# Optimization experiments

Hardware: AMD Instinct MI355X
Metric: run time of the kernel (lower is better)

The kernel has to match this reference:

```python
import jax, jax.numpy as jnp
import numpy as np

B, SEQ, NF = 16, 512, 32
E, HID, PRED = 128, 512, 96
N_FFT, HOP, TOPM = 64, 32, 32
W = SEQ // HOP + 1          # 17 windows (centered STFT)
F = N_FFT // 2 + 1          # 33 onesided freqs
LAM = 0.01                  # sparsity_threshold (softshrink)
SCALE = 0.02


def _hann(n):
    # periodic hann, matches torch.hann_window default
    return 0.5 - 0.5 * jnp.cos(2.0 * jnp.pi * jnp.arange(n) / n)


def _softshrink(v):
    return jnp.sign(v) * jnp.maximum(jnp.abs(v) - LAM, 0.0)


def setup_inputs():
    key = jax.random.key(0)
    ks = jax.random.split(key, 12)
    d = {}
    d['x'] = jax.random.normal(ks[0], (B, SEQ, NF), jnp.float32)
    d['embeddings'] = jax.random.normal(ks[1], (1, E), jnp.float32)
    for nm, k in zip(['Wr', 'Wi', 'Wrl', 'Wil', 'Wrr', 'Wir'], ks[2:8]):
        d[nm] = SCALE * jax.random.normal(k, (W, E, E), jnp.float32)
    d['br'] = SCALE * jax.random.normal(ks[8], (W, E), jnp.float32)
    d['bi'] = SCALE * jax.random.normal(ks[9], (W, E), jnp.float32)
    d['fc_w1'] = SCALE * jax.random.normal(ks[10], (SEQ * E, HID), jnp.float32)
    d['fc_b1'] = jnp.zeros((HID,), jnp.float32)
    d['fc_w2'] = SCALE * jax.random.normal(ks[11], (HID, PRED), jnp.float32)
    d['fc_b2'] = jnp.zeros((PRED,), jnp.float32)
    return d


def _forward(x, embeddings, Wr, Wi, Wrl, Wil, Wrr, Wir, br, bi,
             fc_w1, fc_b1, fc_w2, fc_b2):
    Bq, T, N = x.shape
    # tokenEmb: (B,T,N) -> (B,N,T,E)
    xe = x.transpose(0, 2, 1)[..., None] * embeddings
    bias = xe
    # ---- STFT (centered, reflect pad, hann, onesided) ----
    xt = xe.transpose(0, 1, 3, 2)                      # (B,N,E,T)
    pad = N_FFT // 2
    xp = jnp.pad(xt, ((0, 0), (0, 0), (0, 0), (pad, pad)), mode='reflect')
    win = _hann(N_FFT).astype(x.dtype)
    idx = jnp.arange(W)[:, None] * HOP + jnp.arange(N_FFT)[None, :]  # (W,nfft)
    frames = xp[..., idx] * win                        # (B,N,E,W,nfft)
    spec = jnp.fft.rfft(frames, axis=-1)               # (B,N,E,W,F)
    spec = spec.transpose(0, 1, 3, 4, 2)               # (B,N,W,F,E)
    # ---- top-M frequency select (dim=3) ----
    sm = jnp.moveaxis(spec, 3, -1)                     # (B,N,W,E,F)
    _, top_idx = jax.lax.top_k(jnp.abs(sm), TOPM)      # (B,N,W,E,M)
    vals = jnp.take_along_axis(sm, top_idx, axis=-1)
    xw = jnp.moveaxis(vals, -1, 3)                     # (B,N,W,M,E)
    # ---- per-window complex MLP with left/right neighbor windows ----
    z0 = jnp.zeros_like(xw[:, :, :1])
    xl = jnp.concatenate([z0, xw[:, :, :-1]], axis=2)  # left neighbor (zero at w=0)
    xr = jnp.concatenate([xw[:, :, 1:], z0], axis=2)   # right neighbor (zero at w=W-1)

    def cmul(z, wr, wi):
        re = jnp.einsum('bnwme,wef->bnwmf', z.real, wr) - jnp.einsum('bnwme,wef->bnwmf', z.imag, wi)
        im = jnp.einsum('bnwme,wef->bnwmf', z.imag, wr) + jnp.einsum('bnwme,wef->bnwmf', z.real, wi)
        return re, im

    re_m, im_m = cmul(xw, Wr, Wi)
    re_l, im_l = cmul(xl, Wrl, Wil)
    re_r, im_r = cmul(xr, Wrr, Wir)
    o_re = jax.nn.relu(re_m + re_l + re_r + br[None, None, :, None, :])
    o_im = jax.nn.relu(im_m + im_l + im_r + bi[None, None, :, None, :])
    y = _softshrink(o_re) + 1j * _softshrink(o_im)     # (B,N,W,M,E) complex
    # ---- scatter-pad back to full frequency grid ----
    ym = jnp.moveaxis(y, 3, -1)                        # (B,N,W,E,M)
    K = Bq * N * W * E
    flat_vals = ym.reshape(K, TOPM)
    flat_idx = top_idx.reshape(K, TOPM)
    full = jnp.zeros((K, F), ym.dtype).at[jnp.arange(K)[:, None], flat_idx].set(flat_vals)
    spec_full = jnp.moveaxis(full.reshape(Bq, N, W, E, F), -1, 3)  # (B,N,W,F,E)
    # ---- ISTFT (windowed OLA / window-squared envelope, centered trim) ----
    sf = spec_full.transpose(0, 1, 4, 2, 3)            # (B,N,E,W,F)
    fr = jnp.fft.irfft(sf, n=N_FFT, axis=-1) * win     # (B,N,E,W,nfft)
    L = (W - 1) * HOP + N_FFT
    ola = jnp.zeros((Bq, N, E, L), fr.dtype).at[..., idx].add(fr)
    env = jnp.zeros((L,), win.dtype).at[idx].add(win * win)
    ola = ola / jnp.where(env > 1e-11, env, 1.0)
    xt2 = ola[..., pad:L - pad]                        # (B,N,E,T)
    xo = xt2.transpose(0, 1, 3, 2) + bias              # (B,N,T,E) + residual
    # ---- fc head ----
    h = xo.reshape(Bq, N, T * E)
    h = jax.nn.leaky_relu(h @ fc_w1 + fc_b1, 0.01)
    out = h @ fc_w2 + fc_b2                            # (B,N,PRED)
    return out.transpose(0, 2, 1)                      # (B,PRED,N)


def reference(x, embeddings, Wr, Wi, Wrl, Wil, Wrr, Wir, br, bi,
              fc_w1, fc_b1, fc_w2, fc_b2):
    return _forward(x, embeddings, Wr, Wi, Wrl, Wil, Wrr, Wir, br, bi,
                    fc_w1, fc_b1, fc_w2, fc_b2)
```

## Files before the change

kernel.cpp:

```cpp
#include <hip/hip_runtime.h>
#include <hip/hip_bf16.h>

#define LAM 0.01f

typedef __attribute__((ext_vector_type(8))) short v8s;
typedef __attribute__((ext_vector_type(4))) float v4f;

static __device__ __forceinline__ unsigned short f2bf(float f) {
    union { float f; unsigned int u; } v; v.f = f;
    unsigned int u = v.u;
    u += 0x7fffu + ((u >> 16) & 1u);
    return (unsigned short)(u >> 16);
}
static __device__ __forceinline__ float bf2f(unsigned short h) {
    union { unsigned int u; float f; } c; c.u = ((unsigned int)h) << 16;
    return c.f;
}
static __device__ __forceinline__ unsigned int pkbf(float a, float b) {
    union { __hip_bfloat162 h; unsigned int u; } c;
    c.h = __float22bfloat162_rn(float2{a, b});
    return c.u;
}

static __device__ __forceinline__ void async16(const void* g, void* l) {
    __builtin_amdgcn_global_load_lds(
        (const __attribute__((address_space(1))) unsigned int*)g,
        (__attribute__((address_space(3))) unsigned int*)l, 16, 0, 0);
}

#define OFF_COEF 0ull
#define OFF_AIMG 3411968ull
#define OFF_W1P  70520832ull
#define OFF_HP   137629696ull

__global__ __launch_bounds__(256) void pre_kernel(
    const float* __restrict__ w1, unsigned short* __restrict__ w1p,
    const float* __restrict__ emb,
    const float* __restrict__ Wr, const float* __restrict__ Wi,
    const float* __restrict__ Wrl, const float* __restrict__ Wil,
    const float* __restrict__ Wrr, const float* __restrict__ Wir,
    const float* __restrict__ br, const float* __restrict__ bi,
    float* __restrict__ coef)
{
    if (blockIdx.y == 4) {
        const int bx = blockIdx.x;
        if (bx >= 68) return;
        const int pair = bx * 2 + (threadIdx.x >> 7);
        const int w = pair >> 3, j = pair & 7, e = threadIdx.x & 127;
        float out;
        if (j < 6) {
            const float* Wj;
            switch (j) {
                case 0: Wj = Wr; break; case 1: Wj = Wi; break;
                case 2: Wj = Wrl; break; case 3: Wj = Wil; break;
                case 4: Wj = Wrr; break; default: Wj = Wir; break;
            }
            const float* p = Wj + (size_t)w * 16384 + e;
            float acc = 0.f;
            #pragma unroll 8
            for (int ep = 0; ep < 128; ++ep) acc = fmaf(emb[ep], p[ep * 128], acc);
            out = acc;
        } else if (j == 6) {
            out = br[w * 128 + e] - LAM;
        } else {
            out = bi[w * 128 + e] - LAM;
        }
        coef[((size_t)(w * 128 + e)) * 8 + j] = out;
        return;
    }

    __shared__ float T[32][132];
    const int kb = blockIdx.x, nt = blockIdx.y;
    const int tid = threadIdx.x;

    #pragma unroll
    for (int p = 0; p < 4; ++p) {
        int r = (tid >> 5) + p * 8;
        int c = (tid & 31) * 4;
        float4 v = *(const float4*)&w1[((size_t)(kb * 32 + r)) * 512 + nt * 128 + c];
        T[r][c] = v.x; T[r][c + 1] = v.y; T[r][c + 2] = v.z; T[r][c + 3] = v.w;
    }
    __syncthreads();

    unsigned short* dst = w1p + ((size_t)nt * 2048 + kb) * 4096;
    #pragma unroll
    for (int p = 0; p < 2; ++p) {
        int pos = tid + 256 * p;
        int np = pos >> 2, cs = pos & 3;
        int clog = cs ^ ((np >> 2) & 3);
        unsigned int pk[4];
        #pragma unroll
        for (int j2 = 0; j2 < 4; ++j2)
            pk[j2] = pkbf(T[clog * 8 + j2 * 2][np], T[clog * 8 + j2 * 2 + 1][np]);
        *(uint4*)&dst[pos * 8] = make_uint4(pk[0], pk[1], pk[2], pk[3]);
    }
}

#define MID_ROLL(J0, J1, J2, J3)                                                \
    {                                                                           \
        _Pragma("unroll") for (int e2 = 0; e2 < 2; ++e2)                        \
        _Pragma("unroll") for (int i = 0; i < 4; ++i) {                         \
            roll[e2][J0][i] = fmaf(acc[0][e2][i], win16[0][i], roll[e2][J0][i]);\
            roll[e2][J1][i] = fmaf(acc[1][e2][i], win16[1][i], roll[e2][J1][i]);\
            roll[e2][J2][i] = fmaf(acc[2][e2][i], win16[2][i], roll[e2][J2][i]);\
            roll[e2][J3][i] = fmaf(acc[3][e2][i], win16[3][i], roll[e2][J3][i]);\
        }                                                                       \
    }

#define MID_FLUSH(JJA, JJB)                                                     \
    {                                                                           \
        _Pragma("unroll") for (int i = 0; i < 4; ++i) {                         \
            int tp = 32 * (w - 1) + q * 4 + i;                                  \
            float xb = sig[tp + 32];                                            \
            _Pragma("unroll") for (int e2 = 0; e2 < 2; ++e2) {                  \
                float val = fmaf(roll[e2][JJA][i], renv[0][i], xb * emb2[e2]);  \
                Aimg[cbase[e2] + (size_t)tp * 16384] = f2bf(val);               \
                roll[e2][JJA][i] = 0.f;                                         \
            }                                                                   \
            int tp2 = tp + 16;                                                  \
            float xb2 = sig[tp2 + 32];                                          \
            _Pragma("unroll") for (int e2 = 0; e2 < 2; ++e2) {                  \
                float val = fmaf(roll[e2][JJB][i], renv[1][i], xb2 * emb2[e2]); \
                Aimg[cbase[e2] + (size_t)tp2 * 16384] = f2bf(val);              \
                roll[e2][JJB][i] = 0.f;                                         \
            }                                                                   \
        }                                                                       \
    }

__global__ __launch_bounds__(256) void stftmid_kernel(
    const float* __restrict__ x, const float* __restrict__ emb,
    const float* __restrict__ coef, unsigned short* __restrict__ Aimg)
{
    __shared__ unsigned short M1t[2][64 * 72];
    __shared__ unsigned short Yt[2][128 * 72];
    __shared__ float cosT[64];
    __shared__ float sinT[64];
    __shared__ float2 Vs2[19 * 32];
    __shared__ int Bns[17 * 32];
    __shared__ float sig[576];
    __shared__ float winT[64];
    __shared__ float2 tw[64];
    __shared__ float2 Sbuf[17 * 33];
    __shared__ float absb[17 * 33];

    const int blk = blockIdx.x;
    const int b = blk >> 5, n = blk & 31;
    const int tid = threadIdx.x;
    const int wave = tid >> 6, lane = tid & 63, l15 = lane & 15, q = lane >> 4;
    const float C64 = 0.09817477042468103f;

    if (tid < 64) {
        float ang = (float)tid * C64;
        winT[tid] = 0.5f - 0.5f * cosf(ang);
        tw[tid] = make_float2(cosf(ang), sinf(ang));
        cosT[tid] = __cosf(ang);
        sinT[tid] = __sinf(ang);
        int r = (tid < 32) ? tid : (18 * 32 + tid - 32);
        Vs2[r] = make_float2(0.f, 0.f);
    }
    for (int l = tid; l < 576; l += 256) {
        int t = (l < 32) ? (32 - l) : ((l < 544) ? (l - 32) : (1054 - l));
        sig[l] = x[(size_t)b * 16384 + t * 32 + n];
    }
    __syncthreads();

    for (int task = tid; task < 561; task += 256) {
        int w = task / 33, f = task - w * 33;
        float sr = 0.f, si = 0.f;
        int base = w * 32;
        for (int t = 0; t < 64; ++t) {
            float sw = sig[base + t] * winT[t];
            float2 cs = tw[(f * t) & 63];
            sr = fmaf(sw, cs.x, sr);
            si = fmaf(sw, -cs.y, si);
        }
        Sbuf[task] = make_float2(sr, si);
        absb[task] = sqrtf(fmaf(sr, sr, si * si));
    }
    __syncthreads();

    for (int task = tid; task < 561; task += 256) {
        int w = task / 33, f = task - w * 33;
        float a = absb[task];
        int base = w * 33, rank = 0;
        for (int j = 0; j < 33; ++j) {
            float aj = absb[base + j];
            rank += (aj > a) || (aj == a && j < f);
        }
        if (rank < 32) {
            Vs2[32 + w * 32 + rank] = Sbuf[task];
            Bns[w * 32 + rank] = f;
        }
    }

    float win16[4][4];
    #pragma unroll
    for (int tt = 0; tt < 4; ++tt)
        #pragma unroll
        for (int i = 0; i < 4; ++i) {
            int t = tt * 16 + q * 4 + i;
            win16[tt][i] = 0.5f - 0.5f * __cosf((float)t * C64);
        }
    float renv[2][4];
    #pragma unroll
    for (int hf = 0; hf < 2; ++hf)
        #pragma unroll
        for (int i = 0; i < 4; ++i) {
            int k = hf * 16 + q * 4 + i;
            float w0 = 0.5f - 0.5f * __cosf((float)k * C64);
            float w1v = 0.5f - 0.5f * __cosf((float)(k + 32) * C64);
            renv[hf][i] = 1.0f / (w0 * w0 + w1v * w1v);
        }
    int ebase[2];
    float emb2[2];
    size_t cbase[2];
    const int mt = blk >> 7, mp = blk & 127, s = (mp >> 2) & 3;
    #pragma unroll
    for (int e2 = 0; e2 < 2; ++e2) {
        ebase[e2] = (wave * 2 + e2) * 16 + l15;
        emb2[e2] = emb[ebase[e2]];
        int e = ebase[e2];
        int echunk = e >> 5, clog = (e >> 3) & 3, cs = clog ^ s, el = e & 7;
        cbase[e2] = ((size_t)mt * 2048 + echunk) * 4096 + mp * 32 + cs * 8 + el;
    }

    float roll[2][4][4];
    #pragma unroll
    for (int e2 = 0; e2 < 2; ++e2)
        #pragma unroll
        for (int jj = 0; jj < 4; ++jj)
            #pragma unroll
            for (int i = 0; i < 4; ++i) roll[e2][jj][i] = 0.f;

    const int e1 = tid & 127;
    const int mg = (tid >> 7) << 4;
    const int tM = tid & 63;
    const int kg = wave << 4;

    __syncthreads();

    for (int w = 0; w < 17; ++w) {
        const int buf = w & 1;
        {
            const float4* cf = (const float4*)(coef + ((size_t)(w * 128 + e1)) * 8);
            float4 cA = cf[0];
            float4 cB = cf[1];
            unsigned int rep[8], imp[8];
            #pragma unroll
            for (int j2 = 0; j2 < 8; ++j2) {
                float rev[2], imv[2];
                #pragma unroll
                for (int sdx = 0; sdx < 2; ++sdx) {
                    int m = mg + j2 * 2 + sdx;
                    float2 vm = Vs2[(w + 1) * 32 + m];
                    float2 vl = Vs2[w * 32 + m];
                    float2 vp = Vs2[(w + 2) * 32 + m];
                    float re = cB.z;
                    re = fmaf(vm.x, cA.x, re); re = fmaf(-vm.y, cA.y, re);
                    re = fmaf(vl.x, cA.z, re); re = fmaf(-vl.y, cA.w, re);
                    re = fmaf(vp.x, cB.x, re); re = fmaf(-vp.y, cB.y, re);
                    float im = cB.w;
                    im = fmaf(vm.y, cA.x, im); im = fmaf(vm.x, cA.y, im);
                    im = fmaf(vl.y, cA.z, im); im = fmaf(vl.x, cA.w, im);
                    im = fmaf(vp.y, cB.x, im); im = fmaf(vp.x, cB.y, im);
                    rev[sdx] = fmaxf(re, 0.f);
                    imv[sdx] = fmaxf(im, 0.f);
                }
                rep[j2] = pkbf(rev[0], rev[1]);
                imp[j2] = pkbf(imv[0], imv[1]);
            }
            uint4* dr = (uint4*)&Yt[buf][e1 * 72 + mg];
            dr[0] = make_uint4(rep[0], rep[1], rep[2], rep[3]);
            dr[1] = make_uint4(rep[4], rep[5], rep[6], rep[7]);
            uint4* di = (uint4*)&Yt[buf][e1 * 72 + 32 + mg];
            di[0] = make_uint4(imp[0], imp[1], imp[2], imp[3]);
            di[1] = make_uint4(imp[4], imp[5], imp[6], imp[7]);
        }
        {
            unsigned int mpk[8];
            #pragma unroll
            for (int j2 = 0; j2 < 8; ++j2) {
                float vv[2];
                #pragma unroll
                for (int sdx = 0; sdx < 2; ++sdx) {
                    int k = kg + j2 * 2 + sdx;
                    int m = k & 31;
                    int r = Bns[w * 32 + m];
                    float sc = (r == 0 || r == 32) ? 0.015625f : 0.03125f;
                    int idx = (r * tM) & 63;
                    vv[sdx] = (k < 32) ? (cosT[idx] * sc) : (-sinT[idx] * sc);
                }
                mpk[j2] = pkbf(vv[0], vv[1]);
            }
            uint4* dm = (uint4*)&M1t[buf][tM * 72 + kg];
            dm[0] = make_uint4(mpk[0], mpk[1], mpk[2], mpk[3]);
            dm[1] = make_uint4(mpk[4], mpk[5], mpk[6], mpk[7]);
        }
        __syncthreads();

        v4f acc[4][2];
        #pragma unroll
        for (int tt = 0; tt < 4; ++tt)
            #pragma unroll
            for (int e2 = 0; e2 < 2; ++e2) acc[tt][e2] = (v4f){0.f, 0.f, 0.f, 0.f};
        #pragma unroll
        for (int ks = 0; ks < 2; ++ks) {
            v8s bfr[2];
            #pragma unroll
            for (int e2 = 0; e2 < 2; ++e2)
                bfr[e2] = *(const v8s*)&Yt[buf][ebase[e2] * 72 + ks * 32 + q * 8];
            #pragma unroll
            for (int tt = 0; tt < 4; ++tt) {
                v8s af = *(const v8s*)&M1t[buf][(tt * 16 + l15) * 72 + ks * 32 + q * 8];
                #pragma unroll
                for (int e2 = 0; e2 < 2; ++e2)
                    acc[tt][e2] = __builtin_amdgcn_mfma_f32_16x16x32_bf16(
                        af, bfr[e2], acc[tt][e2], 0, 0, 0);
            }
        }

        if ((w & 1) == 0) {
            MID_ROLL(0, 1, 2, 3);
            if (w > 0) {
                MID_FLUSH(0, 1);
            } else {
                #pragma unroll
                for (int e2 = 0; e2 < 2; ++e2)
                    #pragma unroll
                    for (int i = 0; i < 4; ++i) {
                        roll[e2][0][i] = 0.f; roll[e2][1][i] = 0.f;
                    }
            }
        } else {
            MID_ROLL(2, 3, 0, 1);
            MID_FLUSH(2, 3);
        }
    }
}

__global__ __launch_bounds__(512) void gemm_kernel(
    const unsigned short* __restrict__ Aimg, const unsigned short* __restrict__ w1p,
    unsigned short* __restrict__ hp, int iters, int KS)
{
    __shared__ unsigned short As[3][8192];
    __shared__ unsigned short Bs[3][8192];

    const int gid = blockIdx.x;
    const int xcd = gid & 7;
    const int u = gid >> 3;
    const int KS4 = KS >> 2;
    const int nt2 = (u >= KS4) ? 1 : 0;
    const int vv = u - nt2 * KS4;
    const int pid = vv * 8 + xcd;
    const int ks = pid >> 1;
    const int mt2 = pid & 1;

    const int tid = threadIdx.x;
    const int wave = tid >> 6, lane = tid & 63;
    const int l15 = lane & 15, q = lane >> 4;
    const int kb0 = ks * iters;

    const int isB = wave >> 2;
    const int sub = wave & 3;
    const unsigned short* gsrc = (isB
        ? w1p + ((size_t)(nt2 * 2 + (sub >> 1)) * 2048 + kb0) * 4096
        : Aimg + ((size_t)(mt2 * 2 + (sub >> 1)) * 2048 + kb0) * 4096)
        + (sub & 1) * 2048 + lane * 8;
    const int ldsoff = (sub >> 1) * 4096 + (sub & 1) * 2048;

    v4f acc[4][8];
    #pragma unroll
    for (int mf = 0; mf < 4; ++mf)
        #pragma unroll
        for (int nf = 0; nf < 8; ++nf) acc[mf][nf] = (v4f){0.f, 0.f, 0.f, 0.f};

    {
        unsigned short* dst0 = (isB ? Bs[0] : As[0]) + ldsoff;
        #pragma unroll
        for (int j = 0; j < 4; ++j) async16(gsrc + j * 512, dst0 + j * 512);
        if (iters > 1) {
            const unsigned short* s1 = gsrc + 4096;
            unsigned short* dst1 = (isB ? Bs[1] : As[1]) + ldsoff;
            #pragma unroll
            for (int j = 0; j < 4; ++j) async16(s1 + j * 512, dst1 + j * 512);
        }
    }

    const int wm = wave >> 1, wn = wave & 1;
    const int ca = (q ^ ((l15 >> 2) & 3)) * 8;
    const int rA = (wm >> 1) * 4096 + ((wm & 1) * 64 + l15) * 32 + ca;
    const int rB = wn * 4096 + l15 * 32 + ca;

    for (int it = 0; it < iters; ++it) {
        if (it + 1 < iters) {
            asm volatile("s_waitcnt vmcnt(4)" ::: "memory");
        } else {
            asm volatile("s_waitcnt vmcnt(0)" ::: "memory");
        }
        __builtin_amdgcn_s_barrier();
        __builtin_amdgcn_sched_barrier(0);
        if (it + 2 < iters) {
            const int nb = (it + 2) % 3;
            const unsigned short* src = gsrc + (size_t)(it + 2) * 4096;
            unsigned short* dst = (isB ? Bs[nb] : As[nb]) + ldsoff;
            #pragma unroll
            for (int j = 0; j < 4; ++j) async16(src + j * 512, dst + j * 512);
        }
        const int cur = it % 3;
        v8s af[4], bf[8];
        #pragma unroll
        for (int f = 0; f < 4; ++f) af[f] = *(const v8s*)&As[cur][rA + f * 512];
        #pragma unroll
        for (int nf = 0; nf < 8; ++nf) bf[nf] = *(const v8s*)&Bs[cur][rB + nf * 512];
        #pragma unroll
        for (int mf = 0; mf < 4; ++mf)
            #pragma unroll
            for (int nf = 0; nf < 8; ++nf)
                acc[mf][nf] = __builtin_amdgcn_mfma_f32_16x16x32_bf16(
                    af[mf], bf[nf], acc[mf][nf], 0, 0, 0);
    }

    #pragma unroll
    for (int mf = 0; mf < 4; ++mf)
        #pragma unroll
        for (int nf = 0; nf < 8; ++nf) {
            int row = mt2 * 256 + wm * 64 + mf * 16 + q * 4;
            int col = nt2 * 256 + wn * 128 + nf * 16 + l15;
            unsigned short* dst = hp + ((size_t)row * KS + ks) * 512 + col;
            #pragma unroll
            for (int i = 0; i < 4; ++i)
                dst[(size_t)i * KS * 512] = f2bf(acc[mf][nf][i]);
        }
}

__global__ __launch_bounds__(256) void fc2_kernel(
    const unsigned short* __restrict__ hp, const float* __restrict__ b1,
    const float* __restrict__ w2, const float* __restrict__ b2,
    float* __restrict__ out, int KS)
{
    __shared__ float hbuf[512];
    __shared__ float part[2][96];
    const int row = blockIdx.x;
    const int tid = threadIdx.x;

    const unsigned int* base = (const unsigned int*)(hp + (size_t)row * KS * 512) + tid;
    float a0 = 0.f, a1 = 0.f;
    #pragma unroll 8
    for (int k = 0; k < KS; ++k) {
        unsigned int v = base[k * 256];
        a0 += bf2f((unsigned short)(v & 0xffff));
        a1 += bf2f((unsigned short)(v >> 16));
    }
    float s0 = a0 + b1[tid * 2];
    float s1 = a1 + b1[tid * 2 + 1];
    hbuf[tid * 2]     = (s0 > 0.f) ? s0 : 0.01f * s0;
    hbuf[tid * 2 + 1] = (s1 > 0.f) ? s1 : 0.01f * s1;
    __syncthreads();

    if (tid < 192) {
        const int c = (tid >= 96) ? 1 : 0;
        const int o = tid - 96 * c;
        float a = 0.f;
        #pragma unroll 8
        for (int h = c * 256; h < c * 256 + 256; ++h)
            a = fmaf(hbuf[h], w2[h * 96 + o], a);
        part[c][o] = a;
    }
    __syncthreads();

    if (tid < 96) {
        float a = part[0][tid] + part[1][tid] + b2[tid];
        int b = row >> 5, n = row & 31;
        out[(size_t)b * 3072 + tid * 32 + n] = a;
    }
}

extern "C" void kernel_launch(void* const* d_in, const int* in_sizes, int n_in,
                              void* d_out, int out_size, void* d_ws, size_t ws_size,
                              hipStream_t stream) {
    const float* x   = (const float*)d_in[0];
    const float* emb = (const float*)d_in[1];
    const float* Wr  = (const float*)d_in[2];
    const float* Wi  = (const float*)d_in[3];
    const float* Wrl = (const float*)d_in[4];
    const float* Wil = (const float*)d_in[5];
    const float* Wrr = (const float*)d_in[6];
    const float* Wir = (const float*)d_in[7];
    const float* br  = (const float*)d_in[8];
    const float* bi  = (const float*)d_in[9];
    const float* w1  = (const float*)d_in[10];
    const float* b1  = (const float*)d_in[11];
    const float* w2  = (const float*)d_in[12];
    const float* b2  = (const float*)d_in[13];

    char* ws = (char*)d_ws;
    float* coef          = (float*)(ws + OFF_COEF);
    unsigned short* Aimg = (unsigned short*)(ws + OFF_AIMG);
    unsigned short* w1p  = (unsigned short*)(ws + OFF_W1P);
    unsigned short* hpp  = (unsigned short*)(ws + OFF_HP);

    int KS = 64;
    size_t hp_bytes = (size_t)KS * 512 * 512 * 2;
    if (OFF_HP + hp_bytes > ws_size) {
        KS = 32; hp_bytes = (size_t)KS * 512 * 512 * 2;
    }
    int iters = 2048 / KS;

    pre_kernel<<<dim3(2048, 5), dim3(256), 0, stream>>>(
        w1, w1p, emb, Wr, Wi, Wrl, Wil, Wrr, Wir, br, bi, coef);
    stftmid_kernel<<<dim3(512), dim3(256), 0, stream>>>(x, emb, coef, Aimg);
    gemm_kernel<<<dim3(4 * KS), dim3(512), 0, stream>>>(Aimg, w1p, hpp, iters, KS);
    fc2_kernel<<<dim3(512), dim3(256), 0, stream>>>(hpp, b1, w2, b2, (float*)d_out, KS);
}
```

Measured before the change: 435.2 us.

## Split STFT/top-k into separate kernel and single-buffer mid kernel LDS

Moves the STFT and top-32 frequency selection out of the fused mid kernel into its own kernel, which writes the selected spectrum values and bin indices to workspace. The mid kernel then reloads them. It also drops double-buffering of the Yt/M1t tiles in favour of a trailing barrier each window, and sets launch_bounds(256,4). The goal is to cut LDS and register use so more blocks fit per CU, at the cost of an extra launch, a global round trip, and an extra sync per window.

```diff
diff --git a/kernel.cpp b/kernel.cpp
--- a/kernel.cpp
+++ b/kernel.cpp
@@ -29,6 +29,8 @@
 }
 
 #define OFF_COEF 0ull
+#define OFF_V    69632ull
+#define OFF_BINS 2297856ull
 #define OFF_AIMG 3411968ull
 #define OFF_W1P  70520832ull
 #define OFF_HP   137629696ull
@@ -96,6 +98,62 @@
     }
 }
 
+__global__ __launch_bounds__(256) void stft_kernel(
+    const float* __restrict__ x, float2* __restrict__ V, int* __restrict__ bins)
+{
+    __shared__ float sig[576];
+    __shared__ float winT[64];
+    __shared__ float2 tw[64];
+    __shared__ float2 Sbuf[17 * 33];
+    __shared__ float absb[17 * 33];
+
+    const int blk = blockIdx.x;
+    const int b = blk >> 5, n = blk & 31;
+    const int tid = threadIdx.x;
+    const float C64 = 0.09817477042468103f;
+
+    if (tid < 64) {
+        float ang = (float)tid * C64;
+        winT[tid] = 0.5f - 0.5f * cosf(ang);
+        tw[tid] = make_float2(cosf(ang), sinf(ang));
+    }
+    for (int l = tid; l < 576; l += 256) {
+        int t = (l < 32) ? (32 - l) : ((l < 544) ? (l - 32) : (1054 - l));
+        sig[l] = x[(size_t)b * 16384 + t * 32 + n];
+    }
+    __syncthreads();
+
+    for (int task = tid; task < 561; task += 256) {
+        int w = task / 33, f = task - w * 33;
+        float sr = 0.f, si = 0.f;
+        int base = w * 32;
+        for (int t = 0; t < 64; ++t) {
+            float sw = sig[base + t] * winT[t];
+            float2 cs = tw[(f * t) & 63];
+            sr = fmaf(sw, cs.x, sr);
+            si = fmaf(sw, -cs.y, si);
+        }
+        Sbuf[task] = make_float2(sr, si);
+        absb[task] = sqrtf(fmaf(sr, sr, si * si));
+    }
+    __syncthreads();
+
+    for (int task = tid; task < 561; task += 256) {
+        int w = task / 33, f = task - w * 33;
+        float a = absb[task];
+        int base = w * 33, rank = 0;
+        for (int j = 0; j < 33; ++j) {
+            float aj = absb[base + j];
+            rank += (aj > a) || (aj == a && j < f);
+        }
+        if (rank < 32) {
+            size_t o = ((size_t)blk * 17 + w) * 32 + rank;
+            V[o] = Sbuf[task];
+            bins[o] = f;
+        }
+    }
+}
+
 #define MID_ROLL(J0, J1, J2, J3)                                                \
     {                                                                           \
         _Pragma("unroll") for (int e2 = 0; e2 < 2; ++e2)                        \
@@ -111,14 +169,14 @@
     {                                                                           \
         _Pragma("unroll") for (int i = 0; i < 4; ++i) {                         \
             int tp = 32 * (w - 1) + q * 4 + i;                                  \
-            float xb = sig[tp + 32];                                            \
+            float xb = xs[tp];                                                  \
             _Pragma("unroll") for (int e2 = 0; e2 < 2; ++e2) {                  \
                 float val = fmaf(roll[e2][JJA][i], renv[0][i], xb * emb2[e2]);  \
                 Aimg[cbase[e2] + (size_t)tp * 16384] = f2bf(val);               \
                 roll[e2][JJA][i] = 0.f;                                         \
             }                                                                   \
             int tp2 = tp + 16;                                                  \
-            float xb2 = sig[tp2 + 32];                                          \
+            float xb2 = xs[tp2];                                                \
             _Pragma("unroll") for (int e2 = 0; e2 < 2; ++e2) {                  \
                 float val = fmaf(roll[e2][JJB][i], renv[1][i], xb2 * emb2[e2]); \
                 Aimg[cbase[e2] + (size_t)tp2 * 16384] = f2bf(val);              \
@@ -127,21 +185,18 @@
         }                                                                       \
     }
 
-__global__ __launch_bounds__(256) void stftmid_kernel(
+__global__ __launch_bounds__(256, 4) void mid_kernel(
     const float* __restrict__ x, const float* __restrict__ emb,
-    const float* __restrict__ coef, unsigned short* __restrict__ Aimg)
+    const float* __restrict__ coef, const float2* __restrict__ V,
+    const int* __restrict__ bins, unsigned short* __restrict__ Aimg)
 {
-    __shared__ unsigned short M1t[2][64 * 72];
-    __shared__ unsigned short Yt[2][128 * 72];
+    __shared__ unsigned short M1t[64 * 72];
+    __shared__ unsigned short Yt[128 * 72];
     __shared__ float cosT[64];
     __shared__ float sinT[64];
     __shared__ float2 Vs2[19 * 32];
     __shared__ int Bns[17 * 32];
-    __shared__ float sig[576];
-    __shared__ float winT[64];
-    __shared__ float2 tw[64];
-    __shared__ float2 Sbuf[17 * 33];
-    __shared__ float absb[17 * 33];
+    __shared__ float xs[512];
 
     const int blk = blockIdx.x;
     const int b = blk >> 5, n = blk & 31;
@@ -151,46 +206,18 @@
 
     if (tid < 64) {
         float ang = (float)tid * C64;
-        winT[tid] = 0.5f - 0.5f * cosf(ang);
-        tw[tid] = make_float2(cosf(ang), sinf(ang));
         cosT[tid] = __cosf(ang);
         sinT[tid] = __sinf(ang);
-        int r = (tid < 32) ? tid : (18 * 32 + tid - 32);
-        Vs2[r] = make_float2(0.f, 0.f);
-    }
-    for (int l = tid; l < 576; l += 256) {
-        int t = (l < 32) ? (32 - l) : ((l < 544) ? (l - 32) : (1054 - l));
-        sig[l] = x[(size_t)b * 16384 + t * 32 + n];
-    }
-    __syncthreads();
-
-    for (int task = tid; task < 561; task += 256) {
-        int w = task / 33, f = task - w * 33;
-        float sr = 0.f, si = 0.f;
-        int base = w * 32;
-        for (int t = 0; t < 64; ++t) {
-            float sw = sig[base + t] * winT[t];
-            float2 cs = tw[(f * t) & 63];
-            sr = fmaf(sw, cs.x, sr);
-            si = fmaf(sw, -cs.y, si);
-        }
-        Sbuf[task] = make_float2(sr, si);
-        absb[task] = sqrtf(fmaf(sr, sr, si * si));
-    }
-    __syncthreads();
-
-    for (int task = tid; task < 561; task += 256) {
-        int w = task / 33, f = task - w * 33;
-        float a = absb[task];
-        int base = w * 33, rank = 0;
-        for (int j = 0; j < 33; ++j) {
-            float aj = absb[base + j];
-            rank += (aj > a) || (aj == a && j < f);
-        }
-        if (rank < 32) {
-            Vs2[32 + w * 32 + rank] = Sbuf[task];
-            Bns[w * 32 + rank] = f;
-        }
+    }
+    {
+        const float2* Vg = V + (size_t)blk * 544;
+        const int* Bg = bins + (size_t)blk * 544;
+        for (int i = tid; i < 544; i += 256) { Vs2[32 + i] = Vg[i]; Bns[i] = Bg[i]; }
+        if (tid < 64) {
+            int r = (tid < 32) ? tid : (18 * 32 + tid - 32);
+            Vs2[r] = make_float2(0.f, 0.f);
+        }
+        for (int i = tid; i < 512; i += 256) xs[i] = x[(size_t)b * 16384 + i * 32 + n];
     }
 
     float win16[4][4];
@@ -240,61 +267,63 @@
     __syncthreads();
 
     for (int w = 0; w < 17; ++w) {
-        const int buf = w & 1;
         {
             const float4* cf = (const float4*)(coef + ((size_t)(w * 128 + e1)) * 8);
             float4 cA = cf[0];
             float4 cB = cf[1];
-            unsigned int rep[8], imp[8];
-            #pragma unroll
-            for (int j2 = 0; j2 < 8; ++j2) {
-                float rev[2], imv[2];
+            #pragma unroll
+            for (int half = 0; half < 2; ++half) {
+                unsigned int rep[4], imp[4];
                 #pragma unroll
-                for (int sdx = 0; sdx < 2; ++sdx) {
-                    int m = mg + j2 * 2 + sdx;
-                    float2 vm = Vs2[(w + 1) * 32 + m];
-                    float2 vl = Vs2[w * 32 + m];
-                    float2 vp = Vs2[(w + 2) * 32 + m];
-                    float re = cB.z;
-                    re = fmaf(vm.x, cA.x, re); re = fmaf(-vm.y, cA.y, re);
-                    re = fmaf(vl.x, cA.z, re); re = fmaf(-vl.y, cA.w, re);
-                    re = fmaf(vp.x, cB.x, re); re = fmaf(-vp.y, cB.y, re);
-                    float im = cB.w;
-                    im = fmaf(vm.y, cA.x, im); im = fmaf(vm.x, cA.y, im);
-                    im = fmaf(vl.y, cA.z, im); im = fmaf(vl.x, cA.w, im);
-                    im = fmaf(vp.y, cB.x, im); im = fmaf(vp.x, cB.y, im);
-                    rev[sdx] = fmaxf(re, 0.f);
-                    imv[sdx] = fmaxf(im, 0.f);
+                for (int j2 = 0; j2 < 4; ++j2) {
+                    float rev[2], imv[2];
+                    #pragma unroll
+                    for (int sdx = 0; sdx < 2; ++sdx) {
+                        int m = mg + half * 8 + j2 * 2 + sdx;
+                        float2 vm = Vs2[(w + 1) * 32 + m];
+                        float2 vl = Vs2[w * 32 + m];
+                        float2 vp = Vs2[(w + 2) * 32 + m];
+                        float re = cB.z;
+                        re = fmaf(vm.x, cA.x, re); re = fmaf(-vm.y, cA.y, re);
+                        re = fmaf(vl.x, cA.z, re); re = fmaf(-vl.y, cA.w, re);
+                        re = fmaf(vp.x, cB.x, re); re = fmaf(-vp.y, cB.y, re);
+                        float im = cB.w;
+                        im = fmaf(vm.y, cA.x, im); im = fmaf(vm.x, cA.y, im);
+                        im = fmaf(vl.y, cA.z, im); im = fmaf(vl.x, cA.w, im);
+                        im = fmaf(vp.y, cB.x, im); im = fmaf(vp.x, cB.y, im);
+                        rev[sdx] = fmaxf(re, 0.f);
+                        imv[sdx] = fmaxf(im, 0.f);
+                    }
+                    rep[j2] = pkbf(rev[0], rev[1]);
+                    imp[j2] = pkbf(imv[0], imv[1]);
                 }
-                rep[j2] = pkbf(rev[0], rev[1]);
-                imp[j2] = pkbf(imv[0], imv[1]);
+                ((uint4*)&Yt[e1 * 72 + mg])[half] =
+                    make_uint4(rep[0], rep[1], rep[2], rep[3]);
+                ((uint4*)&Yt[e1 * 72 + 32 + mg])[half] =
+                    make_uint4(imp[0], imp[1], imp[2], imp[3]);
             }
-            uint4* dr = (uint4*)&Yt[buf][e1 * 72 + mg];
-            dr[0] = make_uint4(rep[0], rep[1], rep[2], rep[3]);
-            dr[1] = make_uint4(rep[4], rep[5], rep[6], rep[7]);
-            uint4* di = (uint4*)&Yt[buf][e1 * 72 + 32 + mg];
-            di[0] = make_uint4(imp[0], imp[1], imp[2], imp[3]);
-            di[1] = make_uint4(imp[4], imp[5], imp[6], imp[7]);
         }
         {
-            unsigned int mpk[8];
-            #pragma unroll
-            for (int j2 = 0; j2 < 8; ++j2) {
-                float vv[2];
+            #pragma unroll
+            for (int half = 0; half < 2; ++half) {
+                unsigned int mpk[4];
                 #pragma unroll
-                for (int sdx = 0; sdx < 2; ++sdx) {
-                    int k = kg + j2 * 2 + sdx;
-                    int m = k & 31;
-                    int r = Bns[w * 32 + m];
-                    float sc = (r == 0 || r == 32) ? 0.015625f : 0.03125f;
-                    int idx = (r * tM) & 63;
-                    vv[sdx] = (k < 32) ? (cosT[idx] * sc) : (-sinT[idx] * sc);
+                for (int j2 = 0; j2 < 4; ++j2) {
+                    float vv[2];
+                    #pragma unroll
+                    for (int sdx = 0; sdx < 2; ++sdx) {
+                        int k = kg + half * 8 + j2 * 2 + sdx;
+                        int m = k & 31;
+                        int r = Bns[w * 32 + m];
+                        float sc = (r == 0 || r == 32) ? 0.015625f : 0.03125f;
+                        int idx = (r * tM) & 63;
+                        vv[sdx] = (k < 32) ? (cosT[idx] * sc) : (-sinT[idx] * sc);
+                    }
+                    mpk[j2] = pkbf(vv[0], vv[1]);
                 }
-                mpk[j2] = pkbf(vv[0], vv[1]);
+                ((uint4*)&M1t[tM * 72 + kg])[half] =
+                    make_uint4(mpk[0], mpk[1], mpk[2], mpk[3]);
             }
-            uint4* dm = (uint4*)&M1t[buf][tM * 72 + kg];
-            dm[0] = make_uint4(mpk[0], mpk[1], mpk[2], mpk[3]);
-            dm[1] = make_uint4(mpk[4], mpk[5], mpk[6], mpk[7]);
         }
         __syncthreads();
 
@@ -308,10 +337,10 @@
             v8s bfr[2];
             #pragma unroll
             for (int e2 = 0; e2 < 2; ++e2)
-                bfr[e2] = *(const v8s*)&Yt[buf][ebase[e2] * 72 + ks * 32 + q * 8];
+                bfr[e2] = *(const v8s*)&Yt[ebase[e2] * 72 + ks * 32 + q * 8];
             #pragma unroll
             for (int tt = 0; tt < 4; ++tt) {
-                v8s af = *(const v8s*)&M1t[buf][(tt * 16 + l15) * 72 + ks * 32 + q * 8];
+                v8s af = *(const v8s*)&M1t[(tt * 16 + l15) * 72 + ks * 32 + q * 8];
                 #pragma unroll
                 for (int e2 = 0; e2 < 2; ++e2)
                     acc[tt][e2] = __builtin_amdgcn_mfma_f32_16x16x32_bf16(
@@ -335,6 +364,7 @@
             MID_ROLL(2, 3, 0, 1);
             MID_FLUSH(2, 3);
         }
+        if (w < 16) __syncthreads();
     }
 }
 
@@ -495,6 +525,8 @@
 
     char* ws = (char*)d_ws;
     float* coef          = (float*)(ws + OFF_COEF);
+    float2* V            = (float2*)(ws + OFF_V);
+    int* bins            = (int*)(ws + OFF_BINS);
     unsigned short* Aimg = (unsigned short*)(ws + OFF_AIMG);
     unsigned short* w1p  = (unsigned short*)(ws + OFF_W1P);
     unsigned short* hpp  = (unsigned short*)(ws + OFF_HP);
@@ -508,7 +540,8 @@
 
     pre_kernel<<<dim3(2048, 5), dim3(256), 0, stream>>>(
         w1, w1p, emb, Wr, Wi, Wrl, Wil, Wrr, Wir, br, bi, coef);
-    stftmid_kernel<<<dim3(512), dim3(256), 0, stream>>>(x, emb, coef, Aimg);
+    stft_kernel<<<dim3(512), dim3(256), 0, stream>>>(x, V, bins);
+    mid_kernel<<<dim3(512), dim3(256), 0, stream>>>(x, emb, coef, V, bins, Aimg);
     gemm_kernel<<<dim3(4 * KS), dim3(512), 0, stream>>>(Aimg, w1p, hpp, iters, KS);
     fc2_kernel<<<dim3(512), dim3(256), 0, stream>>>(hpp, b1, w2, b2, (float*)d_out, KS);
 }
```

Measured after the change: 398.8 us. 1.09x faster.

## Move STFT and top-k selection into idle pre_kernel blocks

Applied to the files above, without the earlier changes.

The forward STFT and per-window top-32 frequency ranking move out of the mid kernel into otherwise idle blocks of pre_kernel's y=4 row. Each (b,n) pair is split across two blocks by window halves. Results go to global V/bins buffers that mid_kernel loads, and mid_kernel keeps only a small residual signal buffer. The aim is to overlap this serial per-block work with the w1 repacking and to shorten mid_kernel, at the cost of a global round-trip and extra workspace.

```diff
diff --git a/kernel.cpp b/kernel.cpp
--- a/kernel.cpp
+++ b/kernel.cpp
@@ -29,6 +29,8 @@
 }
 
 #define OFF_COEF 0ull
+#define OFF_V    69632ull
+#define OFF_BINS 2297856ull
 #define OFF_AIMG 3411968ull
 #define OFF_W1P  70520832ull
 #define OFF_HP   137629696ull
@@ -40,38 +42,100 @@
     const float* __restrict__ Wrl, const float* __restrict__ Wil,
     const float* __restrict__ Wrr, const float* __restrict__ Wir,
     const float* __restrict__ br, const float* __restrict__ bi,
-    float* __restrict__ coef)
+    float* __restrict__ coef,
+    const float* __restrict__ x, float2* __restrict__ V, int* __restrict__ bins)
 {
+    __shared__ float T[32][132];
+    __shared__ float sigL[336];
+    __shared__ float winT[64];
+    __shared__ float2 tw[64];
+    __shared__ float2 Sbuf[9 * 33];
+    __shared__ float absb[9 * 33];
+
+    const int tid = threadIdx.x;
+
     if (blockIdx.y == 4) {
         const int bx = blockIdx.x;
-        if (bx >= 68) return;
-        const int pair = bx * 2 + (threadIdx.x >> 7);
-        const int w = pair >> 3, j = pair & 7, e = threadIdx.x & 127;
-        float out;
-        if (j < 6) {
-            const float* Wj;
-            switch (j) {
-                case 0: Wj = Wr; break; case 1: Wj = Wi; break;
-                case 2: Wj = Wrl; break; case 3: Wj = Wil; break;
-                case 4: Wj = Wrr; break; default: Wj = Wir; break;
-            }
-            const float* p = Wj + (size_t)w * 16384 + e;
-            float acc = 0.f;
-            #pragma unroll 8
-            for (int ep = 0; ep < 128; ++ep) acc = fmaf(emb[ep], p[ep * 128], acc);
-            out = acc;
-        } else if (j == 6) {
-            out = br[w * 128 + e] - LAM;
-        } else {
-            out = bi[w * 128 + e] - LAM;
-        }
-        coef[((size_t)(w * 128 + e)) * 8 + j] = out;
+        if (bx < 68) {
+            const int pair = bx * 2 + (tid >> 7);
+            const int w = pair >> 3, j = pair & 7, e = tid & 127;
+            float out;
+            if (j < 6) {
+                const float* Wj;
+                switch (j) {
+                    case 0: Wj = Wr; break; case 1: Wj = Wi; break;
+                    case 2: Wj = Wrl; break; case 3: Wj = Wil; break;
+                    case 4: Wj = Wrr; break; default: Wj = Wir; break;
+                }
+                const float* p = Wj + (size_t)w * 16384 + e;
+                float acc = 0.f;
+                #pragma unroll 8
+                for (int ep = 0; ep < 128; ++ep) acc = fmaf(emb[ep], p[ep * 128], acc);
+                out = acc;
+            } else if (j == 6) {
+                out = br[w * 128 + e] - LAM;
+            } else {
+                out = bi[w * 128 + e] - LAM;
+            }
+            coef[((size_t)(w * 128 + e)) * 8 + j] = out;
+            return;
+        }
+        if (bx < 1024) return;
+        const int blk = bx - 1024;
+        const int bn = blk >> 1, wh = blk & 1;
+        const int b = bn >> 5, n = bn & 31;
+        const int w0 = wh ? 9 : 0;
+        const int nW = wh ? 8 : 9;
+        const int sbase = wh ? 288 : 0;
+        const int slen = wh ? 288 : 320;
+        const float C64 = 0.09817477042468103f;
+
+        if (tid < 64) {
+            float ang = (float)tid * C64;
+            winT[tid] = 0.5f - 0.5f * cosf(ang);
+            tw[tid] = make_float2(cosf(ang), sinf(ang));
+        }
+        for (int l = tid; l < slen; l += 256) {
+            int g = sbase + l;
+            int t = (g < 32) ? (32 - g) : ((g < 544) ? (g - 32) : (1054 - g));
+            sigL[l] = x[(size_t)b * 16384 + t * 32 + n];
+        }
+        __syncthreads();
+
+        const int ntask = nW * 33;
+        for (int task = tid; task < ntask; task += 256) {
+            int wl = task / 33, f = task - wl * 33;
+            float sr = 0.f, si = 0.f;
+            int base = (w0 + wl) * 32 - sbase;
+            for (int t = 0; t < 64; ++t) {
+                float sw = sigL[base + t] * winT[t];
+                float2 cs = tw[(f * t) & 63];
+                sr = fmaf(sw, cs.x, sr);
+                si = fmaf(sw, -cs.y, si);
+            }
+            Sbuf[task] = make_float2(sr, si);
+            absb[task] = sqrtf(fmaf(sr, sr, si * si));
+        }
+        __syncthreads();
+
+        for (int task = tid; task < ntask; task += 256) {
+            int wl = task / 33, f = task - wl * 33;
+            float a = absb[task];
+            int base = wl * 33, rank = 0;
+            for (int j = 0; j < 33; ++j) {
+                float aj = absb[base + j];
+                rank += (aj > a) || (aj == a && j < f);
+            }
+            if (rank < 32) {
+                size_t o = ((size_t)bn * 17 + (w0 + wl)) * 32 + rank;
+                V[o] = Sbuf[task];
+                bins[o] = f;
+            }
+        }
         return;
     }
 
-    __shared__ float T[32][132];
     const int kb = blockIdx.x, nt = blockIdx.y;
-    const int tid = threadIdx.x;
 
     #pragma unroll
     for (int p = 0; p < 4; ++p) {
@@ -111,14 +175,14 @@
     {                                                                           \
         _Pragma("unroll") for (int i = 0; i < 4; ++i) {                         \
             int tp = 32 * (w - 1) + q * 4 + i;                                  \
-            float xb = sig[tp + 32];                                            \
+            float xb = xs[tp];                                                  \
             _Pragma("unroll") for (int e2 = 0; e2 < 2; ++e2) {                  \
                 float val = fmaf(roll[e2][JJA][i], renv[0][i], xb * emb2[e2]);  \
                 Aimg[cbase[e2] + (size_t)tp * 16384] = f2bf(val);               \
                 roll[e2][JJA][i] = 0.f;                                         \
             }                                                                   \
             int tp2 = tp + 16;                                                  \
-            float xb2 = sig[tp2 + 32];                                          \
+            float xb2 = xs[tp2];                                                \
             _Pragma("unroll") for (int e2 = 0; e2 < 2; ++e2) {                  \
                 float val = fmaf(roll[e2][JJB][i], renv[1][i], xb2 * emb2[e2]); \
                 Aimg[cbase[e2] + (size_t)tp2 * 16384] = f2bf(val);              \
@@ -127,9 +191,10 @@
         }                                                                       \
     }
 
-__global__ __launch_bounds__(256) void stftmid_kernel(
+__global__ __launch_bounds__(256) void mid_kernel(
     const float* __restrict__ x, const float* __restrict__ emb,
-    const float* __restrict__ coef, unsigned short* __restrict__ Aimg)
+    const float* __restrict__ coef, const float2* __restrict__ V,
+    const int* __restrict__ bins, unsigned short* __restrict__ Aimg)
 {
     __shared__ unsigned short M1t[2][64 * 72];
     __shared__ unsigned short Yt[2][128 * 72];
@@ -137,11 +202,7 @@
     __shared__ float sinT[64];
     __shared__ float2 Vs2[19 * 32];
     __shared__ int Bns[17 * 32];
-    __shared__ float sig[576];
-    __shared__ float winT[64];
-    __shared__ float2 tw[64];
-    __shared__ float2 Sbuf[17 * 33];
-    __shared__ float absb[17 * 33];
+    __shared__ float xs[512];
 
     const int blk = blockIdx.x;
     const int b = blk >> 5, n = blk & 31;
@@ -151,46 +212,18 @@
 
     if (tid < 64) {
         float ang = (float)tid * C64;
-        winT[tid] = 0.5f - 0.5f * cosf(ang);
-        tw[tid] = make_float2(cosf(ang), sinf(ang));
         cosT[tid] = __cosf(ang);
         sinT[tid] = __sinf(ang);
-        int r = (tid < 32) ? tid : (18 * 32 + tid - 32);
-        Vs2[r] = make_float2(0.f, 0.f);
-    }
-    for (int l = tid; l < 576; l += 256) {
-        int t = (l < 32) ? (32 - l) : ((l < 544) ? (l - 32) : (1054 - l));
-        sig[l] = x[(size_t)b * 16384 + t * 32 + n];
-    }
-    __syncthreads();
-
-    for (int task = tid; task < 561; task += 256) {
-        int w = task / 33, f = task - w * 33;
-        float sr = 0.f, si = 0.f;
-        int base = w * 32;
-        for (int t = 0; t < 64; ++t) {
-            float sw = sig[base + t] * winT[t];
-            float2 cs = tw[(f * t) & 63];
-            sr = fmaf(sw, cs.x, sr);
-            si = fmaf(sw, -cs.y, si);
-        }
-        Sbuf[task] = make_float2(sr, si);
-        absb[task] = sqrtf(fmaf(sr, sr, si * si));
-    }
-    __syncthreads();
-
-    for (int task = tid; task < 561; task += 256) {
-        int w = task / 33, f = task - w * 33;
-        float a = absb[task];
-        int base = w * 33, rank = 0;
-        for (int j = 0; j < 33; ++j) {
-            float aj = absb[base + j];
-            rank += (aj > a) || (aj == a && j < f);
-        }
-        if (rank < 32) {
-            Vs2[32 + w * 32 + rank] = Sbuf[task];
-            Bns[w * 32 + rank] = f;
-        }
+    }
+    {
+        const float2* Vg = V + (size_t)blk * 544;
+        const int* Bg = bins + (size_t)blk * 544;
+        for (int i = tid; i < 544; i += 256) { Vs2[32 + i] = Vg[i]; Bns[i] = Bg[i]; }
+        if (tid < 64) {
+            int r = (tid < 32) ? tid : (18 * 32 + tid - 32);
+            Vs2[r] = make_float2(0.f, 0.f);
+        }
+        for (int i = tid; i < 512; i += 256) xs[i] = x[(size_t)b * 16384 + i * 32 + n];
     }
 
     float win16[4][4];
@@ -495,6 +528,8 @@
 
     char* ws = (char*)d_ws;
     float* coef          = (float*)(ws + OFF_COEF);
+    float2* V            = (float2*)(ws + OFF_V);
+    int* bins            = (int*)(ws + OFF_BINS);
     unsigned short* Aimg = (unsigned short*)(ws + OFF_AIMG);
     unsigned short* w1p  = (unsigned short*)(ws + OFF_W1P);
     unsigned short* hpp  = (unsigned short*)(ws + OFF_HP);
@@ -507,8 +542,8 @@
     int iters = 2048 / KS;
 
     pre_kernel<<<dim3(2048, 5), dim3(256), 0, stream>>>(
-        w1, w1p, emb, Wr, Wi, Wrl, Wil, Wrr, Wir, br, bi, coef);
-    stftmid_kernel<<<dim3(512), dim3(256), 0, stream>>>(x, emb, coef, Aimg);
+        w1, w1p, emb, Wr, Wi, Wrl, Wil, Wrr, Wir, br, bi, coef, x, V, bins);
+    mid_kernel<<<dim3(512), dim3(256), 0, stream>>>(x, emb, coef, V, bins, Aimg);
     gemm_kernel<<<dim3(4 * KS), dim3(512), 0, stream>>>(Aimg, w1p, hpp, iters, KS);
     fc2_kernel<<<dim3(512), dim3(256), 0, stream>>>(hpp, b1, w2, b2, (float*)d_out, KS);
 }
```

After: 374.5 us. 1.16x faster.
